# Optimization experiments

Measured on AMD Instinct MI355X. Metric: run time of the kernel, lower is better.

Reference implementation:

```python
import jax, jax.numpy as jnp
import numpy as np

NUM_LEVELS = 16
FEATURES_PER_LEVEL = 2
LOG2_HASHMAP_SIZE = 19
BASE_RES = 16
FINEST_RES = 2048
N_POINTS = 2097152

_growth = np.exp((np.log(FINEST_RES) - np.log(BASE_RES)) / (NUM_LEVELS - 1))
RESOLUTIONS = np.floor(BASE_RES * _growth ** np.arange(NUM_LEVELS)).astype(np.int64)  # (L,)
TABLE_SIZES = np.minimum(RESOLUTIONS ** 3, 2 ** LOG2_HASHMAP_SIZE).astype(np.int32)   # (L,)
MAX_TABLE_SIZE = 2 ** LOG2_HASHMAP_SIZE

P1, P2, P3 = 73856093, 19349663, 83492791  # spatial hash primes


def setup_inputs() -> dict:
    key = jax.random.key(0)
    k1, k2 = jax.random.split(key)
    coordinates = jax.random.uniform(k1, (N_POINTS, 3), dtype=jnp.float32)
    # keras 'uniform' initializer = U(-0.05, 0.05); tables stacked & zero-padded to max size
    hash_tables = jax.random.uniform(
        k2, (NUM_LEVELS, MAX_TABLE_SIZE, FEATURES_PER_LEVEL),
        minval=-0.05, maxval=0.05, dtype=jnp.float32)
    return {"coordinates": coordinates, "hash_tables": hash_tables}


def reference(coordinates, hash_tables):
    batch_shape = coordinates.shape[:-1]
    coords = coordinates.reshape(-1, 3)  # (N, 3)
    res = jnp.asarray(RESOLUTIONS.astype(np.float32))          # (L,)
    sizes = jnp.asarray(TABLE_SIZES)                            # (L,) int32
    # all levels at once: (L, N, 3)
    grid = jnp.floor(coords[None, :, :] * res[:, None, None]).astype(jnp.int32)
    x, y, t = grid[..., 0], grid[..., 1], grid[..., 2]
    h = (x * np.int32(P1)) ^ (y * np.int32(P2)) ^ (t * np.int32(P3))  # int32 wraparound, like TF
    idx = jnp.abs(h) % sizes[:, None]                           # (L, N)
    feats = jnp.take_along_axis(hash_tables, idx[:, :, None], axis=1)  # (L, N, F)
    out = jnp.transpose(feats, (1, 0, 2)).reshape(coords.shape[0], NUM_LEVELS * FEATURES_PER_LEVEL)
    return out.reshape(*batch_shape, NUM_LEVELS * FEATURES_PER_LEVEL)
```

## Files before the change

### kernel.cpp

```cpp
#include <hip/hip_runtime.h>
#include <stdint.h>


#define TPB 256

typedef float vfloat4 __attribute__((ext_vector_type(4)));
typedef float vfloat2 __attribute__((ext_vector_type(2)));

__device__ __forceinline__ uint32_t hash_idx(float cx, float cy, float cz,
                                             int resi, int siz)
{
    const float rf = (float)resi;
    const int x = (int)floorf(cx * rf);
    const int y = (int)floorf(cy * rf);
    const int z = (int)floorf(cz * rf);
    const uint32_t h = (uint32_t)x * 73856093u
                     ^ (uint32_t)y * 19349663u
                     ^ (uint32_t)z * 83492791u;
    const int32_t hs = (int32_t)h;
    if (siz == (1 << 19)) {
        const uint32_t a = (hs < 0) ? (0u - h) : h;
        return a & 0x7FFFFu;
    } else {
        int32_t a = (hs < 0) ? (int32_t)(0u - h) : hs;
        int32_t r = a % siz;
        if (r < 0) r += siz;
        return (uint32_t)r;
    }
}

#define RESI_LIST {16, 22, 30, 42, 58, 80, 111, 153, \
                   212, 294, 406, 561, 776, 1072, 1482, 2048}
#define SIZ_LIST  {4096, 10648, 27000, 74088, 195112, 512000, \
                   524288, 524288, 524288, 524288, 524288, \
                   524288, 524288, 524288, 524288, 524288}

template<int LV>
__device__ __forceinline__ void gather_body(
    const float* __restrict__ coords,
    const float* __restrict__ tables,
    float2* __restrict__ ws,
    int npts, long long bid2, int t)
{
    constexpr int RESI[16] = RESI_LIST;
    constexpr int SIZ[16] = SIZ_LIST;

    const long long base = bid2 * 2048;
    const float* tab = tables + ((size_t)LV << 20);

    vfloat2 g[8];
#pragma unroll
    for (int j = 0; j < 8; ++j) {
        const long long p = base + j * 256 + t;
        const float cx = coords[3 * p + 0];
        const float cy = coords[3 * p + 1];
        const float cz = coords[3 * p + 2];
        const uint32_t idx = hash_idx(cx, cy, cz, RESI[LV], SIZ[LV]);
        g[j] = *reinterpret_cast<const vfloat2*>(tab + ((size_t)idx << 1));
    }
    float2* wl = ws + (size_t)(LV - 5) * npts + base;
#pragma unroll
    for (int j = 0; j < 8; ++j)
        __builtin_nontemporal_store(g[j],
            reinterpret_cast<vfloat2*>(wl + j * 256 + t));
}

template<int LA, int LB>
__global__ __launch_bounds__(TPB) void hashenc_gather_pair(
    const float* __restrict__ coords,
    const float* __restrict__ tables,
    float2* __restrict__ ws,
    int npts)
{
    const int t = threadIdx.x;
    const long long bid2 = blockIdx.x >> 1;
    if (blockIdx.x & 1)
        gather_body<LB>(coords, tables, ws, npts, bid2, t);
    else
        gather_body<LA>(coords, tables, ws, npts, bid2, t);
}

template<int LV>
__global__ __launch_bounds__(TPB) void hashenc_gather_lv(
    const float* __restrict__ coords,
    const float* __restrict__ tables,
    float2* __restrict__ ws,
    int npts)
{
    gather_body<LV>(coords, tables, ws, npts, (long long)blockIdx.x, threadIdx.x);
}

__global__ __launch_bounds__(TPB) void hashenc_transpose_fused(
    const float* __restrict__ coords,
    const float* __restrict__ tables,
    const float2* __restrict__ ws,
    float* __restrict__ out,
    int npts)
{
    constexpr int RESI[16] = RESI_LIST;
    constexpr int SIZ[16] = SIZ_LIST;

    __shared__ float buf[128 * 33];

    const int t = threadIdx.x;
    const long long pbase = (long long)blockIdx.x * TPB;
    const long long p = pbase + t;

    const float cx = coords[3 * p + 0];
    const float cy = coords[3 * p + 1];
    const float cz = coords[3 * p + 2];

    vfloat2 feat[16];
#pragma unroll
    for (int l = 0; l < 5; ++l) {
        const uint32_t idx = hash_idx(cx, cy, cz, RESI[l], SIZ[l]);
        feat[l] = *reinterpret_cast<const vfloat2*>(
            tables + ((size_t)l << 20) + ((size_t)idx << 1));
    }
#pragma unroll
    for (int l = 5; l < 16; ++l)
        feat[l] = __builtin_nontemporal_load(
            reinterpret_cast<const vfloat2*>(ws + (size_t)(l - 5) * npts + p));

    float* oblk = out + pbase * 32;
#pragma unroll
    for (int h = 0; h < 2; ++h) {
        if ((t >> 7) == h) {
            const int r = t & 127;
#pragma unroll
            for (int l = 0; l < 16; ++l) {
                buf[r * 33 + 2 * l + 0] = feat[l].x;
                buf[r * 33 + 2 * l + 1] = feat[l].y;
            }
        }
        __syncthreads();
#pragma unroll
        for (int k = 0; k < 4; ++k) {
            const int f = k * 1024 + t * 4;
            const int row = f >> 5;
            const int col = f & 31;
            const vfloat4 v = *reinterpret_cast<const vfloat4*>(&buf[row * 33 + col]);
            __builtin_nontemporal_store(v,
                reinterpret_cast<vfloat4*>(&oblk[(long long)h * 4096 + f]));
        }
        __syncthreads();
    }
}

__global__ __launch_bounds__(TPB) void hashenc_kernel(
    const float* __restrict__ coords,
    const float* __restrict__ tables,
    float* __restrict__ out,
    int npts)
{
    constexpr int RESI[16] = RESI_LIST;
    constexpr int SIZ[16] = SIZ_LIST;

    __shared__ float buf[128 * 33];

    const int t = threadIdx.x;
    const long long pbase = (long long)blockIdx.x * TPB;
    const long long p = pbase + t;

    const float cx = coords[3 * p + 0];
    const float cy = coords[3 * p + 1];
    const float cz = coords[3 * p + 2];

    float2 feat[16];
#pragma unroll
    for (int l = 0; l < 16; ++l) {
        const uint32_t idx = hash_idx(cx, cy, cz, RESI[l], SIZ[l]);
        feat[l] = *reinterpret_cast<const float2*>(
            tables + ((size_t)l << 20) + ((size_t)idx << 1));
    }

    float* oblk = out + pbase * 32;
#pragma unroll
    for (int h = 0; h < 2; ++h) {
        if ((t >> 7) == h) {
            const int r = t & 127;
#pragma unroll
            for (int l = 0; l < 16; ++l) {
                buf[r * 33 + 2 * l + 0] = feat[l].x;
                buf[r * 33 + 2 * l + 1] = feat[l].y;
            }
        }
        __syncthreads();
#pragma unroll
        for (int k = 0; k < 4; ++k) {
            const int f = k * 1024 + t * 4;
            const int row = f >> 5;
            const int col = f & 31;
            const vfloat4 v = *reinterpret_cast<const vfloat4*>(&buf[row * 33 + col]);
            __builtin_nontemporal_store(v,
                reinterpret_cast<vfloat4*>(&oblk[(long long)h * 4096 + f]));
        }
        __syncthreads();
    }
}

extern "C" void kernel_launch(void* const* d_in, const int* in_sizes, int n_in,
                              void* d_out, int out_size, void* d_ws, size_t ws_size,
                              hipStream_t stream)
{
    const float* coords = (const float*)d_in[0];
    const float* tables = (const float*)d_in[1];
    float* out = (float*)d_out;
    const int npts = in_sizes[0] / 3;

    const size_t need = (size_t)11 * (size_t)npts * sizeof(float2);
    if (ws_size >= need && (npts % 2048) == 0) {
        float2* ws = (float2*)d_ws;
        const dim3 gp(npts / 1024), g1(npts / 2048), b(TPB);
        hipLaunchKernelGGL((hashenc_gather_pair<5, 6>),   gp, b, 0, stream, coords, tables, ws, npts);
        hipLaunchKernelGGL((hashenc_gather_pair<7, 8>),   gp, b, 0, stream, coords, tables, ws, npts);
        hipLaunchKernelGGL((hashenc_gather_pair<9, 10>),  gp, b, 0, stream, coords, tables, ws, npts);
        hipLaunchKernelGGL((hashenc_gather_pair<11, 12>), gp, b, 0, stream, coords, tables, ws, npts);
        hipLaunchKernelGGL((hashenc_gather_pair<13, 14>), gp, b, 0, stream, coords, tables, ws, npts);
        hipLaunchKernelGGL((hashenc_gather_lv<15>),       g1, b, 0, stream, coords, tables, ws, npts);
        hipLaunchKernelGGL(hashenc_transpose_fused, dim3(npts / TPB), b, 0, stream,
                           coords, tables, (const float2*)d_ws, out, npts);
    } else {
        hipLaunchKernelGGL(hashenc_kernel, dim3(npts / TPB), dim3(TPB), 0, stream,
                           coords, tables, out, npts);
    }
}
```

Measured before the change: 304.1 us.

## Merge per-level gather launches into an 8-way kernel plus a tail kernel

Replaces six gather launches, each covering one or two hash levels, with two launches. The first interleaves levels 5-12 across blocks; the second spreads levels 13-15 over a shared grid, with bounds checks. This cuts launch count and per-launch tail idle time, so more levels are gathered concurrently. The cost is that more hash tables are live in cache at once, which may hurt L2 locality, and some tail blocks do no work.

```diff
diff --git a/kernel.cpp b/kernel.cpp
--- a/kernel.cpp
+++ b/kernel.cpp
@@ -40,12 +40,12 @@
     const float* __restrict__ coords,
     const float* __restrict__ tables,
     float2* __restrict__ ws,
-    int npts, long long bid2, int t)
+    int npts, long long pb, int t)
 {
     constexpr int RESI[16] = RESI_LIST;
     constexpr int SIZ[16] = SIZ_LIST;
 
-    const long long base = bid2 * 2048;
+    const long long base = pb * 2048;
     const float* tab = tables + ((size_t)LV << 20);
 
     vfloat2 g[8];
@@ -65,29 +65,48 @@
             reinterpret_cast<vfloat2*>(wl + j * 256 + t));
 }
 
-template<int LA, int LB>
-__global__ __launch_bounds__(TPB) void hashenc_gather_pair(
+__global__ __launch_bounds__(TPB) void hashenc_gather_8way(
     const float* __restrict__ coords,
     const float* __restrict__ tables,
     float2* __restrict__ ws,
     int npts)
 {
     const int t = threadIdx.x;
-    const long long bid2 = blockIdx.x >> 1;
-    if (blockIdx.x & 1)
-        gather_body<LB>(coords, tables, ws, npts, bid2, t);
-    else
-        gather_body<LA>(coords, tables, ws, npts, bid2, t);
-}
-
-template<int LV>
-__global__ __launch_bounds__(TPB) void hashenc_gather_lv(
+    const int c = blockIdx.x & 7;
+    const long long pb = blockIdx.x >> 3;
+    switch (c) {
+        case 0: gather_body<5>(coords, tables, ws, npts, pb, t); break;
+        case 1: gather_body<6>(coords, tables, ws, npts, pb, t); break;
+        case 2: gather_body<7>(coords, tables, ws, npts, pb, t); break;
+        case 3: gather_body<8>(coords, tables, ws, npts, pb, t); break;
+        case 4: gather_body<9>(coords, tables, ws, npts, pb, t); break;
+        case 5: gather_body<10>(coords, tables, ws, npts, pb, t); break;
+        case 6: gather_body<11>(coords, tables, ws, npts, pb, t); break;
+        case 7: gather_body<12>(coords, tables, ws, npts, pb, t); break;
+    }
+}
+
+__global__ __launch_bounds__(TPB) void hashenc_gather_tail(
     const float* __restrict__ coords,
     const float* __restrict__ tables,
     float2* __restrict__ ws,
     int npts)
 {
-    gather_body<LV>(coords, tables, ws, npts, (long long)blockIdx.x, threadIdx.x);
+    const int t = threadIdx.x;
+    const int c = blockIdx.x & 7;
+    const long long k = blockIdx.x >> 3;
+    const long long npb = npts >> 11;
+    long long pb;
+    switch (c) {
+        case 0: pb = 0 + 3 * k; if (pb < npb) gather_body<13>(coords, tables, ws, npts, pb, t); break;
+        case 1: pb = 1 + 3 * k; if (pb < npb) gather_body<13>(coords, tables, ws, npts, pb, t); break;
+        case 2: pb = 2 + 3 * k; if (pb < npb) gather_body<13>(coords, tables, ws, npts, pb, t); break;
+        case 3: pb = 0 + 3 * k; if (pb < npb) gather_body<14>(coords, tables, ws, npts, pb, t); break;
+        case 4: pb = 1 + 3 * k; if (pb < npb) gather_body<14>(coords, tables, ws, npts, pb, t); break;
+        case 5: pb = 2 + 3 * k; if (pb < npb) gather_body<14>(coords, tables, ws, npts, pb, t); break;
+        case 6: pb = 0 + 2 * k; if (pb < npb) gather_body<15>(coords, tables, ws, npts, pb, t); break;
+        case 7: pb = 1 + 2 * k; if (pb < npb) gather_body<15>(coords, tables, ws, npts, pb, t); break;
+    }
 }
 
 __global__ __launch_bounds__(TPB) void hashenc_transpose_fused(
@@ -211,13 +230,12 @@
     const size_t need = (size_t)11 * (size_t)npts * sizeof(float2);
     if (ws_size >= need && (npts % 2048) == 0) {
         float2* ws = (float2*)d_ws;
-        const dim3 gp(npts / 1024), g1(npts / 2048), b(TPB);
-        hipLaunchKernelGGL((hashenc_gather_pair<5, 6>),   gp, b, 0, stream, coords, tables, ws, npts);
-        hipLaunchKernelGGL((hashenc_gather_pair<7, 8>),   gp, b, 0, stream, coords, tables, ws, npts);
-        hipLaunchKernelGGL((hashenc_gather_pair<9, 10>),  gp, b, 0, stream, coords, tables, ws, npts);
-        hipLaunchKernelGGL((hashenc_gather_pair<11, 12>), gp, b, 0, stream, coords, tables, ws, npts);
-        hipLaunchKernelGGL((hashenc_gather_pair<13, 14>), gp, b, 0, stream, coords, tables, ws, npts);
-        hipLaunchKernelGGL((hashenc_gather_lv<15>),       g1, b, 0, stream, coords, tables, ws, npts);
+        const int npb = npts / 2048;
+        const dim3 gA(npb * 8), gB(((npb + 1) / 2) * 8), b(TPB);
+        hipLaunchKernelGGL(hashenc_gather_8way, gA, b, 0, stream,
+                           coords, tables, ws, npts);
+        hipLaunchKernelGGL(hashenc_gather_tail, gB, b, 0, stream,
+                           coords, tables, ws, npts);
         hipLaunchKernelGGL(hashenc_transpose_fused, dim3(npts / TPB), b, 0, stream,
                            coords, tables, (const float2*)d_ws, out, npts);
     } else {
```

After: 298.8 us. About the same (-1.8%).
